# Performance work log

Measured on AMD Instinct MI355X. Metric: run time of the kernel, lower is better.

Reference implementation:

```python
import jax, jax.numpy as jnp
import numpy as np

N, M, D = 16384, 1024, 1024


def setup_inputs() -> dict:
    key = jax.random.key(0)
    kq, kp = jax.random.split(key)
    query = jax.random.normal(kq, (N, D), dtype=jnp.float32)
    proto = jax.random.normal(kp, (M, D), dtype=jnp.float32)
    return {"query": query, "proto": proto}


def reference(query, proto):
    # Pairwise squared euclidean: ||q||^2 - 2 q.p + ||p||^2  (same math as
    # the expand+pow+sum in compute_euclidean, but without the [N,M,D] blowup).
    q2 = jnp.sum(query * query, axis=-1, keepdims=True)          # [N,1]
    p2 = jnp.sum(proto * proto, axis=-1)                          # [M]
    qp = jnp.einsum('nd,md->nm', query, proto)                    # [N,M]
    dists = q2 - 2.0 * qp + p2[None, :]                           # [N,M]
    # Original applies F.softmax(-dists, dim=1) (named log_p_y but is softmax).
    return jax.nn.softmax(-dists, axis=1)
```

## Files before the change

### kernel.cpp

```cpp
#include <hip/hip_runtime.h>
#include <stdint.h>

#define N_Q 16384
#define M_P 1024
#define D_K 1024

typedef __attribute__((ext_vector_type(8))) __bf16 bf16x8;
typedef __attribute__((ext_vector_type(4))) float floatx4;

#define AS1 __attribute__((address_space(1)))
#define AS3 __attribute__((address_space(3)))

__device__ __forceinline__ unsigned short f2bf(float f) {
    unsigned int u = __float_as_uint(f);
    u += 0x7fffu + ((u >> 16) & 1u);
    return (unsigned short)(u >> 16);
}
__device__ __forceinline__ float bf2f(unsigned short h) {
    return __uint_as_float(((unsigned int)h) << 16);
}

__device__ __forceinline__ void split8(floatx4 f0, floatx4 f1,
                                       bf16x8* ah, bf16x8* al) {
    union { bf16x8 v; unsigned short s[8]; } H, L;
    float e[8] = {f0.x, f0.y, f0.z, f0.w, f1.x, f1.y, f1.z, f1.w};
#pragma unroll
    for (int j = 0; j < 8; ++j) {
        unsigned int u = __float_as_uint(e[j]);
        H.s[j] = (unsigned short)(u >> 16);
        float lo = e[j] - __uint_as_float(u & 0xffff0000u);
        L.s[j] = (unsigned short)(__float_as_uint(lo) >> 16);
    }
    *ah = H.v;
    *al = L.v;
}

__global__ __launch_bounds__(256) void convert_proto_kernel(
    const float* __restrict__ proto, unsigned short* __restrict__ ph,
    unsigned short* __restrict__ pl, float* __restrict__ p2) {
    __shared__ float sred[4];
    int m = blockIdx.x;
    int t = threadIdx.x;
    size_t base4 = (size_t)m * (D_K / 4) + t;
    float4 v = ((const float4*)proto)[base4];
    ushort4 h, l;
    h.x = f2bf(v.x); l.x = f2bf(v.x - bf2f(h.x));
    h.y = f2bf(v.y); l.y = f2bf(v.y - bf2f(h.y));
    h.z = f2bf(v.z); l.z = f2bf(v.z - bf2f(h.z));
    h.w = f2bf(v.w); l.w = f2bf(v.w - bf2f(h.w));
    ((ushort4*)ph)[base4] = h;
    ((ushort4*)pl)[base4] = l;
    float sq = v.x * v.x + v.y * v.y + v.z * v.z + v.w * v.w;
#pragma unroll
    for (int off = 1; off < 64; off <<= 1) sq += __shfl_xor(sq, off);
    if ((t & 63) == 0) sred[t >> 6] = sq;
    __syncthreads();
    if (t == 0) p2[m] = sred[0] + sred[1] + sred[2] + sred[3];
}

__global__ __launch_bounds__(128, 2) void gemm_logits_kernel(
    const float* __restrict__ query,
    const unsigned short* __restrict__ ph, const unsigned short* __restrict__ pl,
    const float* __restrict__ p2, float* __restrict__ out) {
    __shared__ float sAf[128 * 32];
    __shared__ unsigned short sBh[128 * 32];
    __shared__ unsigned short sBl[128 * 32];

    const int tid = threadIdx.x;
    const int wave = tid >> 6;
    const int lane = tid & 63;
    const int b = blockIdx.x;
    const int mt = (b >> 3) & 7;
    const int nt = (b & 7) | ((b >> 6) << 3);
    const int row0 = nt * 128;
    const int col0 = mt * 128;

    const int rlB = lane >> 2;
    const int cioB = (lane & 3) ^ ((lane >> 3) & 3);
    const size_t laneoffB = (size_t)rlB * D_K + cioB * 8;
    const unsigned short* gBh = ph + (size_t)col0 * D_K + laneoffB;
    const unsigned short* gBl = pl + (size_t)col0 * D_K + laneoffB;

    const int rlA = lane >> 3;
    const int cioA = (lane & 7) ^ rlA;
    const float* gA = query + (size_t)(row0 + rlA) * D_K + cioA * 4;

    floatx4 zero = {0.0f, 0.0f, 0.0f, 0.0f};
    floatx4 acc[4][8];
#pragma unroll
    for (int i = 0; i < 4; ++i)
#pragma unroll
        for (int j = 0; j < 8; ++j) acc[i][j] = zero;

    const int rsel = lane & 15;
    const int kq = lane >> 4;
    const int gswB = 4 * rsel + (kq ^ ((rsel >> 1) & 3));
    const int fragoffB = gswB * 8;
    const int pA0 = rsel * 8 + ((2 * kq) ^ (rsel & 7));
    const int pA1 = rsel * 8 + ((2 * kq + 1) ^ (rsel & 7));

    for (int kt = 0; kt < D_K / 32; ++kt) {
        const int kbase = kt * 32;
        if (wave == 0) {
#pragma unroll
            for (int s = 0; s < 8; ++s)
#pragma unroll
                for (int t = 0; t < 2; ++t)
                    __builtin_amdgcn_global_load_lds(
                        (const AS1 unsigned int*)(const void*)(gA + (size_t)(s * 16 + t * 8) * D_K + kbase),
                        (AS3 unsigned int*)(void*)(sAf + s * 512 + t * 256), 16, 0, 0);
        } else {
#pragma unroll
            for (int s = 0; s < 8; ++s) {
                const size_t go = (size_t)(s * 16) * D_K + kbase;
                __builtin_amdgcn_global_load_lds(
                    (const AS1 unsigned int*)(const void*)(gBh + go),
                    (AS3 unsigned int*)(void*)(sBh + s * 512), 16, 0, 0);
                __builtin_amdgcn_global_load_lds(
                    (const AS1 unsigned int*)(const void*)(gBl + go),
                    (AS3 unsigned int*)(void*)(sBl + s * 512), 16, 0, 0);
            }
        }
        __syncthreads();

        bf16x8 ah[4], al[4];
#pragma unroll
        for (int i = 0; i < 4; ++i) {
            const int st = wave * 4 + i;
            floatx4 f0 = *(const floatx4*)(sAf + st * 512 + pA0 * 4);
            floatx4 f1 = *(const floatx4*)(sAf + st * 512 + pA1 * 4);
            split8(f0, f1, &ah[i], &al[i]);
        }
#pragma unroll
        for (int j = 0; j < 8; ++j) {
            const int boff = j * 512 + fragoffB;
            bf16x8 bhj = *(const bf16x8*)(sBh + boff);
            bf16x8 blj = *(const bf16x8*)(sBl + boff);
#pragma unroll
            for (int i = 0; i < 4; ++i) {
                acc[i][j] = __builtin_amdgcn_mfma_f32_16x16x32_bf16(ah[i], bhj, acc[i][j], 0, 0, 0);
                acc[i][j] = __builtin_amdgcn_mfma_f32_16x16x32_bf16(ah[i], blj, acc[i][j], 0, 0, 0);
                acc[i][j] = __builtin_amdgcn_mfma_f32_16x16x32_bf16(al[i], bhj, acc[i][j], 0, 0, 0);
            }
        }
        __syncthreads();
    }

#pragma unroll
    for (int j = 0; j < 8; ++j) {
        const int gc = col0 + j * 16 + rsel;
        const float p2v = p2[gc];
#pragma unroll
        for (int i = 0; i < 4; ++i) {
            const int gr = row0 + wave * 64 + i * 16 + kq * 4;
#pragma unroll
            for (int r = 0; r < 4; ++r) {
                out[(size_t)(gr + r) * M_P + gc] = 2.0f * acc[i][j][r] - p2v;
            }
        }
    }
}

__global__ __launch_bounds__(256) void naive_logits_kernel(
    const float* __restrict__ query, const float* __restrict__ proto,
    float* __restrict__ out) {
    __shared__ float qs[D_K];
    int n = blockIdx.x;
    int t = threadIdx.x;
    ((float4*)qs)[t] = ((const float4*)(query + (size_t)n * D_K))[t];
    __syncthreads();
    float acc[4] = {0.f, 0.f, 0.f, 0.f};
    float pp[4] = {0.f, 0.f, 0.f, 0.f};
    for (int d = 0; d < D_K; d += 4) {
        float4 qv = *(const float4*)(qs + d);
#pragma unroll
        for (int j = 0; j < 4; ++j) {
            const float4 pv = *(const float4*)(proto + (size_t)(t + 256 * j) * D_K + d);
            acc[j] += qv.x * pv.x + qv.y * pv.y + qv.z * pv.z + qv.w * pv.w;
            pp[j] += pv.x * pv.x + pv.y * pv.y + pv.z * pv.z + pv.w * pv.w;
        }
    }
#pragma unroll
    for (int j = 0; j < 4; ++j)
        out[(size_t)n * M_P + t + 256 * j] = 2.0f * acc[j] - pp[j];
}

__global__ __launch_bounds__(256) void softmax_kernel(float* __restrict__ out) {
    const int lane = threadIdx.x & 63;
    int n = blockIdx.x * 4 + (threadIdx.x >> 6);
    for (int it = 0; it < 2; ++it, n += 8192) {
        float* row = out + (size_t)n * M_P;
        floatx4 v[4];
#pragma unroll
        for (int k = 0; k < 4; ++k)
            v[k] = *((const floatx4*)(row + k * 256) + lane);
        float mx = fmaxf(fmaxf(v[0].x, v[0].y), fmaxf(v[0].z, v[0].w));
#pragma unroll
        for (int k = 1; k < 4; ++k)
            mx = fmaxf(mx, fmaxf(fmaxf(v[k].x, v[k].y), fmaxf(v[k].z, v[k].w)));
#pragma unroll
        for (int off = 1; off < 64; off <<= 1) mx = fmaxf(mx, __shfl_xor(mx, off));
        float s = 0.0f;
#pragma unroll
        for (int k = 0; k < 4; ++k) {
            v[k].x = __expf(v[k].x - mx);
            v[k].y = __expf(v[k].y - mx);
            v[k].z = __expf(v[k].z - mx);
            v[k].w = __expf(v[k].w - mx);
            s += v[k].x + v[k].y + v[k].z + v[k].w;
        }
#pragma unroll
        for (int off = 1; off < 64; off <<= 1) s += __shfl_xor(s, off);
        const float inv = 1.0f / s;
#pragma unroll
        for (int k = 0; k < 4; ++k) {
            floatx4 o;
            o.x = v[k].x * inv; o.y = v[k].y * inv;
            o.z = v[k].z * inv; o.w = v[k].w * inv;
            __builtin_nontemporal_store(o, (floatx4*)(row + k * 256) + lane);
        }
    }
}

extern "C" void kernel_launch(void* const* d_in, const int* in_sizes, int n_in,
                              void* d_out, int out_size, void* d_ws, size_t ws_size,
                              hipStream_t stream) {
    const float* query = (const float*)d_in[0];
    const float* proto = (const float*)d_in[1];
    float* out = (float*)d_out;

    const size_t pElems = (size_t)M_P * D_K;
    const size_t needed = pElems * 2 * 2 + M_P * 4;

    if (ws_size >= needed) {
        unsigned short* ph = (unsigned short*)d_ws;
        unsigned short* pl = ph + pElems;
        float* p2 = (float*)(pl + pElems);

        convert_proto_kernel<<<M_P, 256, 0, stream>>>(proto, ph, pl, p2);
        gemm_logits_kernel<<<(N_Q / 128) * (M_P / 128), 128, 0, stream>>>(
            query, ph, pl, p2, out);
    } else {
        naive_logits_kernel<<<N_Q, 256, 0, stream>>>(query, proto, out);
    }
    softmax_kernel<<<2048, 256, 0, stream>>>(out);
}
```

Baseline: 226.1 us.

## Fuse row softmax into GEMM via last-block-per-row-stripe atomic counter

Adds a per-row-stripe atomic counter: the last of the 8 column-tile blocks to finish a 128-row stripe performs the softmax over those rows in place, replacing the separate softmax kernel launch. Counters are zeroed in the proto conversion kernel. This removes one kernel launch and lets the softmax overlap with GEMM tiles still running, but the softmax work is concentrated in 128 blocks of 128 threads, which may give poor parallelism at the tail, and it still rereads the logits from global memory/L2.

Result: slower. 349.8 us (+54.7%).

```diff
diff --git a/kernel.cpp b/kernel.cpp
--- a/kernel.cpp
+++ b/kernel.cpp
@@ -37,10 +37,12 @@
 
 __global__ __launch_bounds__(256) void convert_proto_kernel(
     const float* __restrict__ proto, unsigned short* __restrict__ ph,
-    unsigned short* __restrict__ pl, float* __restrict__ p2) {
+    unsigned short* __restrict__ pl, float* __restrict__ p2,
+    int* __restrict__ cnt) {
     __shared__ float sred[4];
     int m = blockIdx.x;
     int t = threadIdx.x;
+    if (t == 0 && m < 128) cnt[m] = 0;
     size_t base4 = (size_t)m * (D_K / 4) + t;
     float4 v = ((const float4*)proto)[base4];
     ushort4 h, l;
@@ -61,10 +63,12 @@
 __global__ __launch_bounds__(128, 2) void gemm_logits_kernel(
     const float* __restrict__ query,
     const unsigned short* __restrict__ ph, const unsigned short* __restrict__ pl,
-    const float* __restrict__ p2, float* __restrict__ out) {
+    const float* __restrict__ p2, float* __restrict__ out,
+    int* __restrict__ cnt) {
     __shared__ float sAf[128 * 32];
     __shared__ unsigned short sBh[128 * 32];
     __shared__ unsigned short sBl[128 * 32];
+    __shared__ int amlast;
 
     const int tid = threadIdx.x;
     const int wave = tid >> 6;
@@ -157,6 +161,65 @@
             for (int r = 0; r < 4; ++r) {
                 out[(size_t)(gr + r) * M_P + gc] = 2.0f * acc[i][j][r] - p2v;
             }
+        }
+    }
+
+    __threadfence();
+    if (tid == 0) {
+        int prev = atomicAdd(&cnt[nt], 1);
+        amlast = (prev == 7) ? 1 : 0;
+    }
+    __syncthreads();
+    if (!amlast) return;
+    __threadfence();
+
+    float* base = out + (size_t)(row0 + wave * 64) * M_P;
+    for (int rr = 0; rr < 64; rr += 2) {
+        float* r0 = base + (size_t)rr * M_P;
+        float* r1 = r0 + M_P;
+        floatx4 va[4], vb[4];
+#pragma unroll
+        for (int k = 0; k < 4; ++k) {
+            va[k] = *((const floatx4*)r0 + k * 64 + lane);
+            vb[k] = *((const floatx4*)r1 + k * 64 + lane);
+        }
+        float ma = fmaxf(fmaxf(va[0].x, va[0].y), fmaxf(va[0].z, va[0].w));
+        float mb = fmaxf(fmaxf(vb[0].x, vb[0].y), fmaxf(vb[0].z, vb[0].w));
+#pragma unroll
+        for (int k = 1; k < 4; ++k) {
+            ma = fmaxf(ma, fmaxf(fmaxf(va[k].x, va[k].y), fmaxf(va[k].z, va[k].w)));
+            mb = fmaxf(mb, fmaxf(fmaxf(vb[k].x, vb[k].y), fmaxf(vb[k].z, vb[k].w)));
+        }
+#pragma unroll
+        for (int off = 1; off < 64; off <<= 1) {
+            ma = fmaxf(ma, __shfl_xor(ma, off));
+            mb = fmaxf(mb, __shfl_xor(mb, off));
+        }
+        float sa = 0.0f, sb = 0.0f;
+#pragma unroll
+        for (int k = 0; k < 4; ++k) {
+            va[k].x = __expf(va[k].x - ma); va[k].y = __expf(va[k].y - ma);
+            va[k].z = __expf(va[k].z - ma); va[k].w = __expf(va[k].w - ma);
+            sa += va[k].x + va[k].y + va[k].z + va[k].w;
+            vb[k].x = __expf(vb[k].x - mb); vb[k].y = __expf(vb[k].y - mb);
+            vb[k].z = __expf(vb[k].z - mb); vb[k].w = __expf(vb[k].w - mb);
+            sb += vb[k].x + vb[k].y + vb[k].z + vb[k].w;
+        }
+#pragma unroll
+        for (int off = 1; off < 64; off <<= 1) {
+            sa += __shfl_xor(sa, off);
+            sb += __shfl_xor(sb, off);
+        }
+        const float ia = 1.0f / sa, ib = 1.0f / sb;
+#pragma unroll
+        for (int k = 0; k < 4; ++k) {
+            floatx4 oa, ob;
+            oa.x = va[k].x * ia; oa.y = va[k].y * ia;
+            oa.z = va[k].z * ia; oa.w = va[k].w * ia;
+            ob.x = vb[k].x * ib; ob.y = vb[k].y * ib;
+            ob.z = vb[k].z * ib; ob.w = vb[k].w * ib;
+            __builtin_nontemporal_store(oa, (floatx4*)r0 + k * 64 + lane);
+            __builtin_nontemporal_store(ob, (floatx4*)r1 + k * 64 + lane);
         }
     }
 }
@@ -230,18 +293,19 @@
     float* out = (float*)d_out;
 
     const size_t pElems = (size_t)M_P * D_K;
-    const size_t needed = pElems * 2 * 2 + M_P * 4;
+    const size_t needed = pElems * 2 * 2 + M_P * 4 + 128 * 4;
 
     if (ws_size >= needed) {
         unsigned short* ph = (unsigned short*)d_ws;
         unsigned short* pl = ph + pElems;
         float* p2 = (float*)(pl + pElems);
-
-        convert_proto_kernel<<<M_P, 256, 0, stream>>>(proto, ph, pl, p2);
+        int* cnt = (int*)(p2 + M_P);
+
+        convert_proto_kernel<<<M_P, 256, 0, stream>>>(proto, ph, pl, p2, cnt);
         gemm_logits_kernel<<<(N_Q / 128) * (M_P / 128), 128, 0, stream>>>(
-            query, ph, pl, p2, out);
+            query, ph, pl, p2, out, cnt);
     } else {
         naive_logits_kernel<<<N_Q, 256, 0, stream>>>(query, proto, out);
-    }
-    softmax_kernel<<<2048, 256, 0, stream>>>(out);
-}
+        softmax_kernel<<<2048, 256, 0, stream>>>(out);
+    }
+}
```

## Split query into bf16 hi/lo in registers before staging to LDS

Applied to the files above, without the earlier changes.

Query tiles are now loaded by each wave directly into registers, split into bf16 hi/lo parts with byte-permute packing, and written to swizzled LDS buffers. MFMA fragments for A are then read as ready-made bf16x8 vectors, the same way as B. Proto hi/lo loads are split between the two waves. This removes the fp32 LDS staging and the in-loop split at fragment-read time. In exchange the A load becomes synchronous through registers rather than async global-to-LDS, which can expose memory latency.

Result: faster. 212.9 us (-5.9%).

```diff
diff --git a/kernel.cpp b/kernel.cpp
--- a/kernel.cpp
+++ b/kernel.cpp
@@ -7,6 +7,7 @@
 
 typedef __attribute__((ext_vector_type(8))) __bf16 bf16x8;
 typedef __attribute__((ext_vector_type(4))) float floatx4;
+typedef __attribute__((ext_vector_type(4))) unsigned int uint4v;
 
 #define AS1 __attribute__((address_space(1)))
 #define AS3 __attribute__((address_space(3)))
@@ -20,19 +21,24 @@
     return __uint_as_float(((unsigned int)h) << 16);
 }
 
-__device__ __forceinline__ void split8(floatx4 f0, floatx4 f1,
-                                       bf16x8* ah, bf16x8* al) {
-    union { bf16x8 v; unsigned short s[8]; } H, L;
+__device__ __forceinline__ void split_chunk(floatx4 f0, floatx4 f1,
+                                            uint4v* hi, uint4v* lo) {
     float e[8] = {f0.x, f0.y, f0.z, f0.w, f1.x, f1.y, f1.z, f1.w};
-#pragma unroll
-    for (int j = 0; j < 8; ++j) {
-        unsigned int u = __float_as_uint(e[j]);
-        H.s[j] = (unsigned short)(u >> 16);
-        float lo = e[j] - __uint_as_float(u & 0xffff0000u);
-        L.s[j] = (unsigned short)(__float_as_uint(lo) >> 16);
-    }
-    *ah = H.v;
-    *al = L.v;
+    unsigned int hb[4], lb[4];
+#pragma unroll
+    for (int p = 0; p < 4; ++p) {
+        unsigned int u0 = __float_as_uint(e[2 * p]);
+        unsigned int u1 = __float_as_uint(e[2 * p + 1]);
+        hb[p] = __builtin_amdgcn_perm(u1, u0, 0x07060302);
+        float l0 = e[2 * p]     - __uint_as_float(u0 & 0xffff0000u);
+        float l1 = e[2 * p + 1] - __uint_as_float(u1 & 0xffff0000u);
+        lb[p] = __builtin_amdgcn_perm(__float_as_uint(l1), __float_as_uint(l0),
+                                      0x07060302);
+    }
+    uint4v h = {hb[0], hb[1], hb[2], hb[3]};
+    uint4v l = {lb[0], lb[1], lb[2], lb[3]};
+    *hi = h;
+    *lo = l;
 }
 
 __global__ __launch_bounds__(256) void convert_proto_kernel(
@@ -62,7 +68,8 @@
     const float* __restrict__ query,
     const unsigned short* __restrict__ ph, const unsigned short* __restrict__ pl,
     const float* __restrict__ p2, float* __restrict__ out) {
-    __shared__ float sAf[128 * 32];
+    __shared__ unsigned short sAh[128 * 32];
+    __shared__ unsigned short sAl[128 * 32];
     __shared__ unsigned short sBh[128 * 32];
     __shared__ unsigned short sBl[128 * 32];
 
@@ -78,12 +85,15 @@
     const int rlB = lane >> 2;
     const int cioB = (lane & 3) ^ ((lane >> 3) & 3);
     const size_t laneoffB = (size_t)rlB * D_K + cioB * 8;
-    const unsigned short* gBh = ph + (size_t)col0 * D_K + laneoffB;
-    const unsigned short* gBl = pl + (size_t)col0 * D_K + laneoffB;
-
-    const int rlA = lane >> 3;
-    const int cioA = (lane & 7) ^ rlA;
-    const float* gA = query + (size_t)(row0 + rlA) * D_K + cioA * 4;
+    const unsigned short* gB =
+        ((wave == 0) ? ph : pl) + (size_t)col0 * D_K + laneoffB;
+    unsigned short* dstB = (wave == 0) ? sBh : sBl;
+
+    const int rlA = lane >> 2;
+    const int cA = lane & 3;
+    const float* gA = query + (size_t)(row0 + wave * 64 + rlA) * D_K + cA * 8;
+    const int pw = 4 * rlA + (cA ^ ((rlA >> 1) & 3));
+    const int wroff = pw * 8;
 
     floatx4 zero = {0.0f, 0.0f, 0.0f, 0.0f};
     floatx4 acc[4][8];
@@ -94,46 +104,44 @@
 
     const int rsel = lane & 15;
     const int kq = lane >> 4;
-    const int gswB = 4 * rsel + (kq ^ ((rsel >> 1) & 3));
-    const int fragoffB = gswB * 8;
-    const int pA0 = rsel * 8 + ((2 * kq) ^ (rsel & 7));
-    const int pA1 = rsel * 8 + ((2 * kq + 1) ^ (rsel & 7));
+    const int gsw = 4 * rsel + (kq ^ ((rsel >> 1) & 3));
+    const int fragoff = gsw * 8;
 
     for (int kt = 0; kt < D_K / 32; ++kt) {
         const int kbase = kt * 32;
-        if (wave == 0) {
-#pragma unroll
-            for (int s = 0; s < 8; ++s)
-#pragma unroll
-                for (int t = 0; t < 2; ++t)
-                    __builtin_amdgcn_global_load_lds(
-                        (const AS1 unsigned int*)(const void*)(gA + (size_t)(s * 16 + t * 8) * D_K + kbase),
-                        (AS3 unsigned int*)(void*)(sAf + s * 512 + t * 256), 16, 0, 0);
-        } else {
-#pragma unroll
-            for (int s = 0; s < 8; ++s) {
-                const size_t go = (size_t)(s * 16) * D_K + kbase;
-                __builtin_amdgcn_global_load_lds(
-                    (const AS1 unsigned int*)(const void*)(gBh + go),
-                    (AS3 unsigned int*)(void*)(sBh + s * 512), 16, 0, 0);
-                __builtin_amdgcn_global_load_lds(
-                    (const AS1 unsigned int*)(const void*)(gBl + go),
-                    (AS3 unsigned int*)(void*)(sBl + s * 512), 16, 0, 0);
-            }
+#pragma unroll
+        for (int s = 0; s < 8; ++s)
+            __builtin_amdgcn_global_load_lds(
+                (const AS1 unsigned int*)(const void*)(gB + (size_t)(s * 16) * D_K + kbase),
+                (AS3 unsigned int*)(void*)(dstB + s * 512), 16, 0, 0);
+
+        floatx4 f0[4], f1[4];
+#pragma unroll
+        for (int s = 0; s < 4; ++s) {
+            const float* p = gA + (size_t)(s * 16) * D_K + kbase;
+            f0[s] = *(const floatx4*)p;
+            f1[s] = *(const floatx4*)(p + 4);
+        }
+#pragma unroll
+        for (int s = 0; s < 4; ++s) {
+            uint4v hi, lo;
+            split_chunk(f0[s], f1[s], &hi, &lo);
+            const int off = (wave * 4 + s) * 512 + wroff;
+            *(uint4v*)(sAh + off) = hi;
+            *(uint4v*)(sAl + off) = lo;
         }
         __syncthreads();
 
         bf16x8 ah[4], al[4];
 #pragma unroll
         for (int i = 0; i < 4; ++i) {
-            const int st = wave * 4 + i;
-            floatx4 f0 = *(const floatx4*)(sAf + st * 512 + pA0 * 4);
-            floatx4 f1 = *(const floatx4*)(sAf + st * 512 + pA1 * 4);
-            split8(f0, f1, &ah[i], &al[i]);
+            const int aoff = (wave * 4 + i) * 512 + fragoff;
+            ah[i] = *(const bf16x8*)(sAh + aoff);
+            al[i] = *(const bf16x8*)(sAl + aoff);
         }
 #pragma unroll
         for (int j = 0; j < 8; ++j) {
-            const int boff = j * 512 + fragoffB;
+            const int boff = j * 512 + fragoff;
             bf16x8 bhj = *(const bf16x8*)(sBh + boff);
             bf16x8 blj = *(const bf16x8*)(sBl + boff);
 #pragma unroll
@@ -193,7 +201,7 @@
         floatx4 v[4];
 #pragma unroll
         for (int k = 0; k < 4; ++k)
-            v[k] = *((const floatx4*)(row + k * 256) + lane);
+            v[k] = *((const floatx4*)row + k * 64 + lane);
         float mx = fmaxf(fmaxf(v[0].x, v[0].y), fmaxf(v[0].z, v[0].w));
 #pragma unroll
         for (int k = 1; k < 4; ++k)
@@ -217,7 +225,7 @@
             floatx4 o;
             o.x = v[k].x * inv; o.y = v[k].y * inv;
             o.z = v[k].z * inv; o.w = v[k].w * inv;
-            __builtin_nontemporal_store(o, (floatx4*)(row + k * 256) + lane);
+            __builtin_nontemporal_store(o, (floatx4*)row + k * 64 + lane);
         }
     }
 }
```
